# Performance work log

Hardware: AMD Instinct MI355X
Metric: run time of the kernel (lower is better)

The kernel has to match this reference:

```python
import jax, jax.numpy as jnp
import numpy as np

MIN_D, MAX_D = 0.1, 1.0
KSIZE = 5


def gaussian_kernel(ksize):
    sigma = ksize / 6.0
    x = jnp.arange(ksize, dtype=jnp.float32) - ksize // 2
    k1 = jnp.exp(-0.5 * x ** 2 / sigma ** 2)
    k1 = k1 / k1.sum()
    return (k1[:, None] * k1[None, :])[None, None]  # [1,1,k,k]


def setup_inputs() -> dict:
    key = jax.random.key(0)
    k1, k2 = jax.random.split(key)
    B, H, W = 8, 512, 512
    TH = TW = 512
    contrast_map = jax.random.normal(k1, (B, 1, H, W), dtype=jnp.float32)
    # uniform [0,1) randoms replacing the per-sample torch.rand calls
    rand_offsets = jax.random.uniform(k2, (B, TH, TW, 4, 2), dtype=jnp.float32)
    return {
        "contrast_map": contrast_map,
        "rand_offsets": rand_offsets,
        "smoothing_kernel": gaussian_kernel(KSIZE),
        "target_height": TH,
        "target_width": TW,
    }


def reference(contrast_map, rand_offsets, smoothing_kernel, target_height, target_width):
    B, _, H, W = contrast_map.shape
    # per-sample min-max normalization to [0,1]
    mn = contrast_map.min(axis=(1, 2, 3), keepdims=True)
    mx = contrast_map.max(axis=(1, 2, 3), keepdims=True)
    norm = jnp.where(mx > mn, (contrast_map - mn) / (mx - mn), jnp.zeros_like(contrast_map))
    # gaussian smoothing, same padding
    pad = KSIZE // 2
    smoothed = jax.lax.conv_general_dilated(
        norm, smoothing_kernel, window_strides=(1, 1),
        padding=[(pad, pad), (pad, pad)],
        dimension_numbers=("NCHW", "OIHW", "NCHW"))
    # contrast -> density: min_d + (max_d-min_d) * sqrt(c)
    density = MIN_D + (MAX_D - MIN_D) * jnp.sqrt(smoothed)  # [B,1,H,W]

    # nearest-index lookup:  h_idx = floor(i*H/TH) clamped
    hi = jnp.minimum((jnp.arange(target_height) * H) // target_height, H - 1)
    wi = jnp.minimum((jnp.arange(target_width) * W) // target_width, W - 1)
    local = density[:, 0][:, hi][:, :, wi]  # [B,TH,TW]

    # per-pixel sample count: >0.7 -> 4, >0.4 -> 2, else 1
    num_samples = jnp.where(local > 0.7, 4, jnp.where(local > 0.4, 2, 1))  # int [B,TH,TW]

    yb = jnp.linspace(-1.0, 1.0, target_height)
    xb = jnp.linspace(-1.0, 1.0, target_width)
    base = jnp.stack(jnp.broadcast_arrays(yb[:, None], xb[None, :]), axis=-1)  # [TH,TW,2] (y,x)
    cell = jnp.array([2.0 / target_height, 2.0 / target_width], dtype=jnp.float32)
    off = (rand_offsets - 0.5) * cell * 0.8  # [B,TH,TW,4,2]
    use_off = (num_samples > 1)[..., None, None]  # single-sample pixels use the base coord
    coords = base[None, :, :, None, :] + jnp.where(use_off, off, 0.0)  # [B,TH,TW,4,2]

    slot = jnp.arange(4)
    valid = slot[None, None, None, :] < num_samples[..., None]  # [B,TH,TW,4]
    weights = jnp.where(valid, local[..., None] / num_samples[..., None], 0.0)  # [B,TH,TW,4]
    return coords, weights, density
```

## Files before the change

### kernel.cpp

```cpp
#include <hip/hip_runtime.h>

static constexpr int B = 8, Himg = 512, Wimg = 512, TH = 512, TW = 512;
static constexpr int BPB = 32;

typedef float f4 __attribute__((ext_vector_type(4)));
typedef float f2 __attribute__((ext_vector_type(2)));

__global__ __launch_bounds__(256) void minmax_kernel(const float* __restrict__ cm,
                                                     float* __restrict__ wsmin,
                                                     float* __restrict__ wsmax) {
    int b   = blockIdx.x / BPB;
    int blk = blockIdx.x % BPB;
    const f4* p = (const f4*)(cm + (size_t)b * Himg * Wimg);
    float mn = 3.4e38f, mx = -3.4e38f;
    int base = blk * 2048;
    #pragma unroll
    for (int k = 0; k < 8; ++k) {
        f4 v = p[base + k * 256 + threadIdx.x];
        mn = fminf(mn, fminf(fminf(v.x, v.y), fminf(v.z, v.w)));
        mx = fmaxf(mx, fmaxf(fmaxf(v.x, v.y), fmaxf(v.z, v.w)));
    }
    #pragma unroll
    for (int off = 32; off; off >>= 1) {
        mn = fminf(mn, __shfl_xor(mn, off));
        mx = fmaxf(mx, __shfl_xor(mx, off));
    }
    __shared__ float smn[4], smx[4];
    int wave = threadIdx.x >> 6, lane = threadIdx.x & 63;
    if (lane == 0) { smn[wave] = mn; smx[wave] = mx; }
    __syncthreads();
    if (threadIdx.x == 0) {
        mn = fminf(fminf(smn[0], smn[1]), fminf(smn[2], smn[3]));
        mx = fmaxf(fmaxf(smx[0], smx[1]), fmaxf(smx[2], smx[3]));
        wsmin[b * BPB + blk] = mn;
        wsmax[b * BPB + blk] = mx;
    }
}

__global__ __launch_bounds__(256) void fused_kernel(const float* __restrict__ cm,
                                                    const float* __restrict__ kern,
                                                    const float* __restrict__ wsmin,
                                                    const float* __restrict__ wsmax,
                                                    const float* __restrict__ rnd,
                                                    float* __restrict__ coords,
                                                    float* __restrict__ weights,
                                                    float* __restrict__ dens) {
    __shared__ double tile[36][37];
    __shared__ double kd[25];
    __shared__ float dsm[1024];

    int tid = threadIdx.x;
    int b = blockIdx.z;
    int bx = blockIdx.x * 32, by = blockIdx.y * 32;

    if (tid < 25) kd[tid] = (double)kern[tid];

    float mnf = 3.4e38f, mxf = -3.4e38f;
    #pragma unroll
    for (int k = 0; k < BPB; ++k) {
        mnf = fminf(mnf, wsmin[b * BPB + k]);
        mxf = fmaxf(mxf, wsmax[b * BPB + k]);
    }
    bool ok = mxf > mnf;
    double mn = (double)mnf;
    double inv = ok ? (1.0 / ((double)mxf - mn)) : 0.0;

    const float* img = cm + (size_t)b * Himg * Wimg;
    for (int idx = tid; idx < 36 * 36; idx += 256) {
        int r = idx / 36, c = idx % 36;
        int gy = by + r - 2, gx = bx + c - 2;
        double v = 0.0;
        if (gy >= 0 && gy < Himg && gx >= 0 && gx < Wimg)
            v = ((double)img[gy * Wimg + gx] - mn) * inv;
        tile[r][c] = v;
    }
    __syncthreads();

    for (int p = tid; p < 32 * 32; p += 256) {
        int oy = p >> 5, ox = p & 31;
        double s = 0.0;
        #pragma unroll
        for (int dy = 0; dy < 5; ++dy)
            #pragma unroll
            for (int dx = 0; dx < 5; ++dx)
                s += tile[oy + dy][ox + dx] * kd[dy * 5 + dx];
        double D = 0.1 + 0.9 * sqrt(s);
        int code = D > 0.7 ? 2 : (D > 0.4 ? 1 : 0);
        unsigned u = (__float_as_uint((float)D) & ~3u) | (unsigned)code;
        float enc = __uint_as_float(u);
        dsm[p] = enc;
        dens[(size_t)b * Himg * Wimg + (size_t)(by + oy) * Wimg + (bx + ox)] = enc;
    }
    __syncthreads();

    const float cy = (2.0f / TH) * 0.8f;
    const float cx = (2.0f / TW) * 0.8f;
    int lane = tid & 63, wv = tid >> 6;
    #pragma unroll
    for (int k = 0; k < 8; ++k) {
        int row = k * 4 + wv;
        int gy = by + row;
        int gx = bx + (lane >> 1);
        int h = lane & 1;

        float local = dsm[row * 32 + (lane >> 1)];
        int code = __float_as_uint(local) & 3;
        int num = 1 << code;
        bool useoff = num > 1;

        float yb = -1.0f + gy * (2.0f / (TH - 1));
        float xb = -1.0f + gx * (2.0f / (TW - 1));

        size_t f4i = 2 * ((size_t)b * (Himg * Wimg) + (size_t)gy * Wimg + bx) + lane;
        f4 r = ((const f4*)rnd)[f4i];
        f4 c;
        c.x = yb + (useoff ? (r.x - 0.5f) * cy : 0.0f);
        c.y = xb + (useoff ? (r.y - 0.5f) * cx : 0.0f);
        c.z = yb + (useoff ? (r.z - 0.5f) * cy : 0.0f);
        c.w = xb + (useoff ? (r.w - 0.5f) * cx : 0.0f);
        ((f4*)coords)[f4i] = c;

        float invw = local * __uint_as_float(0x3f800000u - ((unsigned)code << 23));
        f2 w;
        if (h == 0) {
            w.x = invw;
            w.y = (num > 1) ? invw : 0.0f;
        } else {
            float v = (num > 3) ? invw : 0.0f;
            w.x = v;
            w.y = v;
        }
        ((f2*)weights)[f4i] = w;
    }
}

extern "C" void kernel_launch(void* const* d_in, const int* in_sizes, int n_in,
                              void* d_out, int out_size, void* d_ws, size_t ws_size,
                              hipStream_t stream) {
    const float* cm   = (const float*)d_in[0];
    const float* rnd  = (const float*)d_in[1];
    const float* kern = (const float*)d_in[2];
    float* out     = (float*)d_out;
    float* coords  = out;
    float* weights = out + (size_t)B * TH * TW * 8;
    float* dens    = weights + (size_t)B * TH * TW * 4;
    float* wsmin   = (float*)d_ws;
    float* wsmax   = wsmin + B * BPB;

    minmax_kernel<<<B * BPB, 256, 0, stream>>>(cm, wsmin, wsmax);
    dim3 gridF(Wimg / 32, Himg / 32, B);
    fused_kernel<<<gridF, 256, 0, stream>>>(cm, kern, wsmin, wsmax, rnd,
                                            coords, weights, dens);
}
```

Before: 47.54 us.

## Compute smoothing in fp32 with register row reuse and fp64 fallback near thresholds

```diff
diff --git a/kernel.cpp b/kernel.cpp
--- a/kernel.cpp
+++ b/kernel.cpp
@@ -45,15 +45,15 @@
                                                     float* __restrict__ coords,
                                                     float* __restrict__ weights,
                                                     float* __restrict__ dens) {
-    __shared__ double tile[36][37];
-    __shared__ double kd[25];
+    __shared__ float tile[36][37];
+    __shared__ float kf[25];
     __shared__ float dsm[1024];
 
     int tid = threadIdx.x;
     int b = blockIdx.z;
     int bx = blockIdx.x * 32, by = blockIdx.y * 32;
 
-    if (tid < 25) kd[tid] = (double)kern[tid];
+    if (tid < 25) kf[tid] = kern[tid];
 
     float mnf = 3.4e38f, mxf = -3.4e38f;
     #pragma unroll
@@ -64,32 +64,67 @@
     bool ok = mxf > mnf;
     double mn = (double)mnf;
     double inv = ok ? (1.0 / ((double)mxf - mn)) : 0.0;
+    float mnf32 = mnf;
+    float invf32 = (float)inv;
 
     const float* img = cm + (size_t)b * Himg * Wimg;
     for (int idx = tid; idx < 36 * 36; idx += 256) {
         int r = idx / 36, c = idx % 36;
         int gy = by + r - 2, gx = bx + c - 2;
-        double v = 0.0;
+        float v = 0.0f;
         if (gy >= 0 && gy < Himg && gx >= 0 && gx < Wimg)
-            v = ((double)img[gy * Wimg + gx] - mn) * inv;
+            v = ok ? (img[gy * Wimg + gx] - mnf32) * invf32 : 0.0f;
         tile[r][c] = v;
     }
     __syncthreads();
 
-    for (int p = tid; p < 32 * 32; p += 256) {
-        int oy = p >> 5, ox = p & 31;
-        double s = 0.0;
+    {
+        int ox = tid & 31;
+        int oy0 = (tid >> 5) << 2;
+        float acc[4] = {0.f, 0.f, 0.f, 0.f};
         #pragma unroll
-        for (int dy = 0; dy < 5; ++dy)
+        for (int yy = 0; yy < 8; ++yy) {
+            float rv[5];
             #pragma unroll
-            for (int dx = 0; dx < 5; ++dx)
-                s += tile[oy + dy][ox + dx] * kd[dy * 5 + dx];
-        double D = 0.1 + 0.9 * sqrt(s);
-        int code = D > 0.7 ? 2 : (D > 0.4 ? 1 : 0);
-        unsigned u = (__float_as_uint((float)D) & ~3u) | (unsigned)code;
-        float enc = __uint_as_float(u);
-        dsm[p] = enc;
-        dens[(size_t)b * Himg * Wimg + (size_t)(by + oy) * Wimg + (bx + ox)] = enc;
+            for (int dx = 0; dx < 5; ++dx) rv[dx] = tile[oy0 + yy][ox + dx];
+            #pragma unroll
+            for (int r = 0; r < 4; ++r) {
+                int dy = yy - r;
+                if (dy >= 0 && dy < 5) {
+                    #pragma unroll
+                    for (int dx = 0; dx < 5; ++dx)
+                        acc[r] = fmaf(rv[dx], kf[dy * 5 + dx], acc[r]);
+                }
+            }
+        }
+        #pragma unroll
+        for (int r = 0; r < 4; ++r) {
+            int oy = oy0 + r;
+            float D32 = 0.1f + 0.9f * sqrtf(fmaxf(acc[r], 0.0f));
+            float Dout = D32;
+            int code;
+            if (fabsf(D32 - 0.7f) < 1e-4f || fabsf(D32 - 0.4f) < 1e-4f) {
+                double s64 = 0.0;
+                #pragma unroll
+                for (int dy = 0; dy < 5; ++dy)
+                    for (int dx = 0; dx < 5; ++dx) {
+                        int gy = by + oy + dy - 2, gx = bx + ox + dx - 2;
+                        double v = 0.0;
+                        if (gy >= 0 && gy < Himg && gx >= 0 && gx < Wimg)
+                            v = ((double)img[gy * Wimg + gx] - mn) * inv;
+                        s64 += v * (double)kern[dy * 5 + dx];
+                    }
+                double D64 = 0.1 + 0.9 * sqrt(s64);
+                code = D64 > 0.7 ? 2 : (D64 > 0.4 ? 1 : 0);
+                Dout = (float)D64;
+            } else {
+                code = D32 > 0.7f ? 2 : (D32 > 0.4f ? 1 : 0);
+            }
+            unsigned u = (__float_as_uint(Dout) & ~3u) | (unsigned)code;
+            float enc = __uint_as_float(u);
+            dsm[oy * 32 + ox] = enc;
+            dens[(size_t)b * Himg * Wimg + (size_t)(by + oy) * Wimg + (bx + ox)] = enc;
+        }
     }
     __syncthreads();
 
```

Result: slower. 49.27 us (+3.6%).
